# Kernel tuning notes

Hardware: AMD Instinct MI355X
Metric: run time of the kernel (lower is better)

The kernel has to match this reference:

```python
import jax, jax.numpy as jnp
import numpy as np
from jax import lax

BATCH = 524288
N_LINKS = 8   # body 0 = fixed base, bodies 1..7 have revolute joints
N_DOFS = 7
G = 9.81      # base linear acceleration z-component encodes gravity

def _skew(v):
    x, y, z = v[..., 0], v[..., 1], v[..., 2]
    o = jnp.zeros_like(x)
    return jnp.stack([jnp.stack([o, -z, y], -1),
                      jnp.stack([z, o, -x], -1),
                      jnp.stack([-y, x, o], -1)], -2)

def _rodrigues(axis, theta):
    # rotation about unit axis by theta; broadcasts axis[...,3] with theta[...]
    K = _skew(axis)
    s = jnp.sin(theta)[..., None, None]
    c = jnp.cos(theta)[..., None, None]
    I = jnp.eye(3, dtype=jnp.result_type(theta))
    return I + s * K + (1.0 - c) * (K @ K)

def setup_inputs():
    key = jax.random.key(0)
    ks = jax.random.split(key, 10)
    q = jax.random.normal(ks[0], (BATCH, N_DOFS), jnp.float32)
    qd = jax.random.normal(ks[1], (BATCH, N_DOFS), jnp.float32)
    qdd_des = jax.random.normal(ks[2], (BATCH, N_DOFS), jnp.float32)
    # fixed (URDF) joint transforms: valid random rotations + link-offset translations
    ax = jax.random.normal(ks[3], (N_LINKS, 3), jnp.float32)
    ax = ax / jnp.linalg.norm(ax, axis=-1, keepdims=True)
    ang = jax.random.uniform(ks[4], (N_LINKS,), jnp.float32, -1.0, 1.0)
    rot_fix = _rodrigues(ax, ang)
    trans_fix = jax.random.uniform(ks[5], (N_LINKS, 3), jnp.float32, -0.25, 0.25)
    # single-coordinate joint axes with signs, as in URDF revolute joints
    joint_axes = jnp.asarray([[0, 0, 1], [0, 1, 0], [0, 0, 1], [0, -1, 0],
                              [0, 0, 1], [0, 1, 0], [0, 0, 1]], jnp.float32)
    mass = jax.random.uniform(ks[6], (N_LINKS,), jnp.float32, 0.5, 4.0)
    com = 0.05 * jax.random.normal(ks[7], (N_LINKS, 3), jnp.float32)
    A = 0.1 * jax.random.normal(ks[8], (N_LINKS, 3, 3), jnp.float32)
    inertia = A @ jnp.swapaxes(A, -1, -2) + 0.05 * jnp.eye(3, dtype=jnp.float32)
    damping = jax.random.uniform(ks[9], (N_DOFS,), jnp.float32, 0.01, 0.2)
    return dict(q=q, qd=qd, qdd_des=qdd_des, rot_fix=rot_fix, trans_fix=trans_fix,
                joint_axes=joint_axes, mass=mass, com=com, inertia=inertia, damping=damping)

def reference(q, qd, qdd_des, rot_fix, trans_fix, joint_axes, mass, com, inertia, damping):
    # Batched recursive Newton-Euler inverse dynamics over a serial chain,
    # matching DifferentiableRobotModel.compute_inverse_dynamics (gravity+damping on).
    B, D = q.shape
    # joint pose of body i(=dof j+1): rotation = rot_fix[i] @ R(axis_j, q_j), translation = trans_fix[i]
    Rq = _rodrigues(joint_axes[None, :, :], q)                     # [B,D,3,3]
    R = jnp.einsum('dij,bdjk->dbik', rot_fix[1:], Rq)              # [D,B,3,3]
    p = trans_fix[1:]                                              # [D,3]
    jv = qd.T[:, :, None] * joint_axes[:, None, :]                 # [D,B,3] joint angular vel
    ja = qdd_des.T[:, :, None] * joint_axes[:, None, :]            # [D,B,3] joint angular acc

    z = jnp.zeros((B, 3), q.dtype)
    base_acc_lin = z.at[:, 2].set(G)

    # forward pass: propagate spatial velocity/acceleration root -> leaf
    def fwd_step(carry, xs):
        vl, va, al, aa = carry
        Ri, pi, jvi, jai = xs
        Rt = jnp.swapaxes(Ri, -1, -2)
        pinv = -jnp.einsum('bij,j->bi', Rt, pi)
        # SpatialMotionVec.transform with inverse joint pose (Rt, pinv)
        va_n = jnp.einsum('bij,bj->bi', Rt, va)
        vl_n = jnp.einsum('bij,bj->bi', Rt, vl) + jnp.cross(pinv, va_n)
        va_i = va_n + jvi
        vl_i = vl_n
        aa_n = jnp.einsum('bij,bj->bi', Rt, aa)
        al_n = jnp.einsum('bij,bj->bi', Rt, al) + jnp.cross(pinv, aa_n)
        # acc = parent_acc(transformed) + joint_acc + vel x joint_vel (joint_vel.lin = 0)
        aa_i = aa_n + jai + jnp.cross(va_i, jvi)
        al_i = al_n + jnp.cross(vl_i, jvi)
        new = (vl_i, va_i, al_i, aa_i)
        return new, new

    _, (vl, va, al, aa) = lax.scan(fwd_step, (z, z, base_acc_lin, z), (R, p, jv, ja))

    # spatial inertia (about body frame origin) acting on motion vectors
    m = mass[1:, None, None]                                       # [D,1,1]
    mc = mass[1:, None] * com[1:]                                  # [D,3]
    cs = _skew(com[1:])
    Io = inertia[1:] + mass[1:, None, None] * (cs @ jnp.swapaxes(cs, -1, -2))

    def imul(lin, ang):
        return (m * lin + jnp.cross(ang, mc[:, None, :]),
                jnp.einsum('dij,dbj->dbi', Io, ang) + jnp.cross(mc[:, None, :], lin))

    Ia_l, Ia_a = imul(al, aa)
    Iv_l, Iv_a = imul(vl, va)
    # f = I*acc + vel x* (I*vel)
    f_l = Ia_l + jnp.cross(va, Iv_l)
    f_a = Ia_a + jnp.cross(va, Iv_a) + jnp.cross(vl, Iv_l)

    # backward pass: accumulate forces leaf -> root; tau_j = f.ang . axis_j
    def bwd_step(carry, xs):
        cl, ca = carry
        fl, fa, Ri, pi, axi = xs
        tl = fl + cl
        ta = fa + ca
        tau = jnp.einsum('bi,i->b', ta, axi)
        # SpatialForceVec.transform with joint pose (Ri, pi)
        nl = jnp.einsum('bij,bj->bi', Ri, tl)
        na = jnp.einsum('bij,bj->bi', Ri, ta) + jnp.cross(pi[None, :], nl)
        return (nl, na), tau

    _, taus = lax.scan(bwd_step, (z, z), (f_l, f_a, R, p, joint_axes), reverse=True)
    return jnp.swapaxes(taus, 0, 1) + damping[None, :] * qd        # [B,D]
```

## Files before the change

kernel.cpp:

```cpp
#include <hip/hip_runtime.h>

#define NDOF 7
#define BLK 256
#define CST_STRIDE 24
#define CST_TOT (NDOF * CST_STRIDE)

struct V3 { float x, y, z; };
__device__ __forceinline__ V3 operator+(V3 a, V3 b) { return {a.x + b.x, a.y + b.y, a.z + b.z}; }
__device__ __forceinline__ V3 operator-(V3 a, V3 b) { return {a.x - b.x, a.y - b.y, a.z - b.z}; }
__device__ __forceinline__ V3 operator*(float s, V3 a) { return {s * a.x, s * a.y, s * a.z}; }
__device__ __forceinline__ V3 cross(V3 a, V3 b) {
    return {a.y * b.z - a.z * b.y, a.z * b.x - a.x * b.z, a.x * b.y - a.y * b.x};
}
__device__ __forceinline__ float dot(V3 a, V3 b) { return a.x * b.x + a.y * b.y + a.z * b.z; }

__global__ void rnea_prep(const float* __restrict__ rot_fix,
                          const float* __restrict__ trans_fix,
                          const float* __restrict__ mass_g,
                          const float* __restrict__ com_g,
                          const float* __restrict__ inertia_g,
                          const float* __restrict__ damping_g,
                          float* __restrict__ cst) {
    const int d = threadIdx.x;
    if (d >= NDOF) return;
    float* o = cst + d * CST_STRIDE;
    const float* F = rot_fix + (1 + d) * 9;
#pragma unroll
    for (int j = 0; j < 3; j++)
#pragma unroll
        for (int i = 0; i < 3; i++) o[j * 3 + i] = F[i * 3 + j];
#pragma unroll
    for (int i = 0; i < 3; i++) o[9 + i] = trans_fix[(1 + d) * 3 + i];
    const float m = mass_g[1 + d];
    const float c0 = com_g[(1 + d) * 3 + 0];
    const float c1 = com_g[(1 + d) * 3 + 1];
    const float c2 = com_g[(1 + d) * 3 + 2];
    const float* I = inertia_g + (1 + d) * 9;
    o[12] = I[0] + m * (c1 * c1 + c2 * c2);
    o[13] = I[1] - m * c0 * c1;
    o[14] = I[2] - m * c0 * c2;
    o[15] = I[4] + m * (c0 * c0 + c2 * c2);
    o[16] = I[5] - m * c1 * c2;
    o[17] = I[8] + m * (c0 * c0 + c1 * c1);
    o[18] = m;
    o[19] = m * c0;
    o[20] = m * c1;
    o[21] = m * c2;
    o[22] = damping_g[d];
    o[23] = 0.f;
}

template <int AX>
__device__ __forceinline__ void make_R(V3 Fc0, V3 Fc1, V3 Fc2, float s, float c,
                                       V3& R0, V3& R1, V3& R2) {
    if (AX == 0) {
        R0 = c * Fc0 + s * Fc1;
        R1 = c * Fc1 - s * Fc0;
        R2 = Fc2;
    } else if (AX == 1) {
        R0 = c * Fc0 - s * Fc2;
        R1 = Fc1;
        R2 = s * Fc0 + c * Fc2;
    } else {
        R0 = c * Fc0 + s * Fc2;
        R1 = Fc1;
        R2 = c * Fc2 - s * Fc0;
    }
}

template <int AX>
__device__ __forceinline__ void fwd_step(const float* __restrict__ C, float s, float c,
                                         float qd, float qdd, V3& vl, V3& va, V3& al,
                                         V3& aa, V3& fl, V3& fa) {
    const V3 Fc0{C[0], C[1], C[2]};
    const V3 Fc1{C[3], C[4], C[5]};
    const V3 Fc2{C[6], C[7], C[8]};
    const V3 p{C[9], C[10], C[11]};
    const float I00 = C[12], I01 = C[13], I02 = C[14], I11 = C[15], I12 = C[16], I22 = C[17];
    const float m = C[18];
    const V3 mc{C[19], C[20], C[21]};

    V3 R0, R1, R2;
    make_R<AX>(Fc0, Fc1, Fc2, s, c, R0, R1, R2);

    V3 w1 = vl + cross(va, p);
    V3 w2 = al + cross(aa, p);
    V3 nvl{dot(R0, w1), dot(R1, w1), dot(R2, w1)};
    V3 nva{dot(R0, va), dot(R1, va), dot(R2, va)};
    V3 nal{dot(R0, w2), dot(R1, w2), dot(R2, w2)};
    V3 naa{dot(R0, aa), dot(R1, aa), dot(R2, aa)};

    if (AX == 0) {
        va = {nva.x, nva.y, nva.z + qd};
        aa = {naa.x + va.y * qd, naa.y - va.x * qd, naa.z + qdd};
        vl = nvl;
        al = {nal.x + vl.y * qd, nal.y - vl.x * qd, nal.z};
    } else if (AX == 1) {
        va = {nva.x, nva.y + qd, nva.z};
        aa = {naa.x - va.z * qd, naa.y + qdd, naa.z + va.x * qd};
        vl = nvl;
        al = {nal.x - vl.z * qd, nal.y, nal.z + vl.x * qd};
    } else {
        va = {nva.x, nva.y - qd, nva.z};
        aa = {naa.x + va.z * qd, naa.y - qdd, naa.z - va.x * qd};
        vl = nvl;
        al = {nal.x + vl.z * qd, nal.y, nal.z - vl.x * qd};
    }

    V3 Ial = m * al + cross(aa, mc);
    V3 Iaa = V3{I00 * aa.x + I01 * aa.y + I02 * aa.z,
                I01 * aa.x + I11 * aa.y + I12 * aa.z,
                I02 * aa.x + I12 * aa.y + I22 * aa.z} + cross(mc, al);
    V3 Ivl = m * vl + cross(va, mc);
    V3 Iva = V3{I00 * va.x + I01 * va.y + I02 * va.z,
                I01 * va.x + I11 * va.y + I12 * va.z,
                I02 * va.x + I12 * va.y + I22 * va.z} + cross(mc, vl);
    fl = Ial + cross(va, Ivl);
    fa = Iaa + cross(va, Iva) + cross(vl, Ivl);
}

template <int AX>
__device__ __forceinline__ float bwd_core(const float* __restrict__ C, float s, float c,
                                          V3 fl, V3 fa, V3& cl, V3& ca) {
    const V3 Fc0{C[0], C[1], C[2]};
    const V3 Fc1{C[3], C[4], C[5]};
    const V3 Fc2{C[6], C[7], C[8]};
    const V3 p{C[9], C[10], C[11]};

    V3 tl = fl + cl;
    V3 ta = fa + ca;
    float tau;
    if (AX == 0) tau = ta.z;
    else if (AX == 1) tau = ta.y;
    else tau = -ta.y;

    V3 R0, R1, R2;
    make_R<AX>(Fc0, Fc1, Fc2, s, c, R0, R1, R2);
    V3 nl = tl.x * R0 + tl.y * R1 + tl.z * R2;
    V3 na = ta.x * R0 + ta.y * R1 + ta.z * R2 + cross(p, nl);
    cl = nl;
    ca = na;
    return tau;
}

__global__ __launch_bounds__(BLK) void rnea_main(
    const float* __restrict__ q_g, const float* __restrict__ qd_g,
    const float* __restrict__ qdd_g, const float* __restrict__ cst,
    float* __restrict__ out, int nbatch) {
    const int t = threadIdx.x;
    const int row = blockIdx.x * BLK + t;
    const int rowc = row < nbatch ? row : (nbatch - 1);
    const size_t go = (size_t)rowc * NDOF;

    float q[NDOF], qd[NDOF], qdd[NDOF], ss[NDOF], cc[NDOF];
#pragma unroll
    for (int d = 0; d < NDOF; d++) q[d] = q_g[go + d];
#pragma unroll
    for (int d = 0; d < NDOF; d++) qd[d] = qd_g[go + d];
#pragma unroll
    for (int d = 0; d < NDOF; d++) qdd[d] = qdd_g[go + d];
#pragma unroll
    for (int d = 0; d < NDOF; d++) { ss[d] = __sinf(q[d]); cc[d] = __cosf(q[d]); }

    V3 vl{0.f, 0.f, 0.f}, va{0.f, 0.f, 0.f}, al{0.f, 0.f, 9.81f}, aa{0.f, 0.f, 0.f};
    V3 fl0, fa0, fl1, fa1, fl2, fa2, fl3, fa3, fl4, fa4, fl5, fa5, fl6, fa6;

    fwd_step<0>(cst + 0 * CST_STRIDE, ss[0], cc[0], qd[0], qdd[0], vl, va, al, aa, fl0, fa0);
    fwd_step<1>(cst + 1 * CST_STRIDE, ss[1], cc[1], qd[1], qdd[1], vl, va, al, aa, fl1, fa1);
    fwd_step<0>(cst + 2 * CST_STRIDE, ss[2], cc[2], qd[2], qdd[2], vl, va, al, aa, fl2, fa2);
    fwd_step<2>(cst + 3 * CST_STRIDE, ss[3], cc[3], qd[3], qdd[3], vl, va, al, aa, fl3, fa3);
    fwd_step<0>(cst + 4 * CST_STRIDE, ss[4], cc[4], qd[4], qdd[4], vl, va, al, aa, fl4, fa4);
    fwd_step<1>(cst + 5 * CST_STRIDE, ss[5], cc[5], qd[5], qdd[5], vl, va, al, aa, fl5, fa5);
    fwd_step<0>(cst + 6 * CST_STRIDE, ss[6], cc[6], qd[6], qdd[6], vl, va, al, aa, fl6, fa6);

    V3 cl{0.f, 0.f, 0.f}, ca{0.f, 0.f, 0.f};
    float tau[NDOF];
    tau[6] = bwd_core<0>(cst + 6 * CST_STRIDE, ss[6], cc[6], fl6, fa6, cl, ca);
    tau[5] = bwd_core<1>(cst + 5 * CST_STRIDE, ss[5], cc[5], fl5, fa5, cl, ca);
    tau[4] = bwd_core<0>(cst + 4 * CST_STRIDE, ss[4], cc[4], fl4, fa4, cl, ca);
    tau[3] = bwd_core<2>(cst + 3 * CST_STRIDE, ss[3], cc[3], fl3, fa3, cl, ca);
    tau[2] = bwd_core<0>(cst + 2 * CST_STRIDE, ss[2], cc[2], fl2, fa2, cl, ca);
    tau[1] = bwd_core<1>(cst + 1 * CST_STRIDE, ss[1], cc[1], fl1, fa1, cl, ca);
    tau[0] = bwd_core<0>(cst + 0 * CST_STRIDE, ss[0], cc[0], fl0, fa0, cl, ca);

    if (row < nbatch) {
#pragma unroll
        for (int d = 0; d < NDOF; d++)
            out[go + d] = tau[d] + cst[d * CST_STRIDE + 22] * qd[d];
    }
}

extern "C" void kernel_launch(void* const* d_in, const int* in_sizes, int n_in,
                              void* d_out, int out_size, void* d_ws, size_t ws_size,
                              hipStream_t stream) {
    const float* q = (const float*)d_in[0];
    const float* qd = (const float*)d_in[1];
    const float* qdd = (const float*)d_in[2];
    const float* rot_fix = (const float*)d_in[3];
    const float* trans_fix = (const float*)d_in[4];
    const float* mass = (const float*)d_in[6];
    const float* com = (const float*)d_in[7];
    const float* inertia = (const float*)d_in[8];
    const float* damping = (const float*)d_in[9];
    float* out = (float*)d_out;
    float* cst = (float*)d_ws;

    const int n_elem = in_sizes[0];
    const int B = n_elem / NDOF;
    const int grid = (B + BLK - 1) / BLK;

    rnea_prep<<<1, 64, 0, stream>>>(rot_fix, trans_fix, mass, com, inertia, damping, cst);
    rnea_main<<<grid, BLK, 0, stream>>>(q, qd, qdd, cst, out, B);
}
```

Before: 134.5 us.

## Stage per-row inputs and outputs through shared memory with coalesced float4 copies

Each block now loads its contiguous slab of q, qd and qdd into shared memory using float4 vector loads, then each thread reads its 7-element row from LDS. Outputs are written back to shared memory and stored with coalesced float4 writes. This replaces the strided 7-float per-thread global accesses, which coalesce poorly, at the cost of about 21 KB of LDS per block, extra barriers, and stride-7 LDS reads.

```diff
diff --git a/kernel.cpp b/kernel.cpp
--- a/kernel.cpp
+++ b/kernel.cpp
@@ -4,6 +4,8 @@
 #define BLK 256
 #define CST_STRIDE 24
 #define CST_TOT (NDOF * CST_STRIDE)
+#define BELEM (BLK * NDOF)
+#define BVEC (BELEM / 4)
 
 struct V3 { float x, y, z; };
 __device__ __forceinline__ V3 operator+(V3 a, V3 b) { return {a.x + b.x, a.y + b.y, a.z + b.z}; }
@@ -147,20 +149,51 @@
     const float* __restrict__ q_g, const float* __restrict__ qd_g,
     const float* __restrict__ qdd_g, const float* __restrict__ cst,
     float* __restrict__ out, int nbatch) {
+    __shared__ __align__(16) float sQ[BELEM];
+    __shared__ __align__(16) float sQd[BELEM];
+    __shared__ __align__(16) float sQdd[BELEM];
     const int t = threadIdx.x;
-    const int row = blockIdx.x * BLK + t;
-    const int rowc = row < nbatch ? row : (nbatch - 1);
-    const size_t go = (size_t)rowc * NDOF;
-
-    float q[NDOF], qd[NDOF], qdd[NDOF], ss[NDOF], cc[NDOF];
-#pragma unroll
-    for (int d = 0; d < NDOF; d++) q[d] = q_g[go + d];
-#pragma unroll
-    for (int d = 0; d < NDOF; d++) qd[d] = qd_g[go + d];
-#pragma unroll
-    for (int d = 0; d < NDOF; d++) qdd[d] = qdd_g[go + d];
-#pragma unroll
-    for (int d = 0; d < NDOF; d++) { ss[d] = __sinf(q[d]); cc[d] = __cosf(q[d]); }
+    const int row0 = blockIdx.x * BLK;
+    const size_t base = (size_t)row0 * NDOF;
+    const bool full = (row0 + BLK) <= nbatch;
+
+    if (full) {
+        const float4* gq = reinterpret_cast<const float4*>(q_g + base);
+        const float4* gqd = reinterpret_cast<const float4*>(qd_g + base);
+        const float4* gqdd = reinterpret_cast<const float4*>(qdd_g + base);
+        float4* s4q = reinterpret_cast<float4*>(sQ);
+        float4* s4qd = reinterpret_cast<float4*>(sQd);
+        float4* s4qdd = reinterpret_cast<float4*>(sQdd);
+#pragma unroll
+        for (int i = 0; i < 2; i++) {
+            const int idx = t + i * BLK;
+            if (idx < BVEC) {
+                s4q[idx] = gq[idx];
+                s4qd[idx] = gqd[idx];
+                s4qdd[idx] = gqdd[idx];
+            }
+        }
+    } else {
+        const int totalE = nbatch * NDOF;
+        for (int i = t; i < BELEM; i += BLK) {
+            const size_t gi = base + i;
+            const bool in = gi < (size_t)totalE;
+            sQ[i] = in ? q_g[gi] : 0.f;
+            sQd[i] = in ? qd_g[gi] : 0.f;
+            sQdd[i] = in ? qdd_g[gi] : 0.f;
+        }
+    }
+    __syncthreads();
+
+    float qd[NDOF], qdd[NDOF], ss[NDOF], cc[NDOF];
+#pragma unroll
+    for (int d = 0; d < NDOF; d++) {
+        const float qv = sQ[t * NDOF + d];
+        ss[d] = __sinf(qv);
+        cc[d] = __cosf(qv);
+        qd[d] = sQd[t * NDOF + d];
+        qdd[d] = sQdd[t * NDOF + d];
+    }
 
     V3 vl{0.f, 0.f, 0.f}, va{0.f, 0.f, 0.f}, al{0.f, 0.f, 9.81f}, aa{0.f, 0.f, 0.f};
     V3 fl0, fa0, fl1, fa1, fl2, fa2, fl3, fa3, fl4, fa4, fl5, fa5, fl6, fa6;
@@ -183,10 +216,26 @@
     tau[1] = bwd_core<1>(cst + 1 * CST_STRIDE, ss[1], cc[1], fl1, fa1, cl, ca);
     tau[0] = bwd_core<0>(cst + 0 * CST_STRIDE, ss[0], cc[0], fl0, fa0, cl, ca);
 
-    if (row < nbatch) {
-#pragma unroll
-        for (int d = 0; d < NDOF; d++)
-            out[go + d] = tau[d] + cst[d * CST_STRIDE + 22] * qd[d];
+    __syncthreads();
+#pragma unroll
+    for (int d = 0; d < NDOF; d++)
+        sQ[t * NDOF + d] = tau[d] + cst[d * CST_STRIDE + 22] * qd[d];
+    __syncthreads();
+
+    if (full) {
+        const float4* s4 = reinterpret_cast<const float4*>(sQ);
+        float4* g4 = reinterpret_cast<float4*>(out + base);
+#pragma unroll
+        for (int i = 0; i < 2; i++) {
+            const int idx = t + i * BLK;
+            if (idx < BVEC) g4[idx] = s4[idx];
+        }
+    } else {
+        const int totalE = nbatch * NDOF;
+        for (int i = t; i < BELEM; i += BLK) {
+            const size_t gi = base + i;
+            if (gi < (size_t)totalE) out[gi] = sQ[i];
+        }
     }
 }
 
```

New measurement: 141.0 us. 1.05x slower.

## Process two rows per thread with packed f32x2 math and LDS-parked forces

Applied to the files above, without the earlier changes.

Each thread now handles two batch rows using float2 ext vectors, so the arithmetic can map to packed FP32 instructions. Per-link forces for the first five links are parked in shared memory instead of registers, and the forward and backward passes become non-unrolled loops. This lowers register pressure and code size. Constants are staged in LDS and loaded as float4, and q/qd are reloaded and sin/cos recomputed in the backward pass. It trades extra LDS traffic, recomputation and loop overhead for packed math and lower register use.

```diff
diff --git a/kernel.cpp b/kernel.cpp
--- a/kernel.cpp
+++ b/kernel.cpp
@@ -1,18 +1,26 @@
 #include <hip/hip_runtime.h>
 
 #define NDOF 7
-#define BLK 256
+#define NPARK 5
+#define BLK 128
+#define RPB 256
 #define CST_STRIDE 24
 #define CST_TOT (NDOF * CST_STRIDE)
-
-struct V3 { float x, y, z; };
-__device__ __forceinline__ V3 operator+(V3 a, V3 b) { return {a.x + b.x, a.y + b.y, a.z + b.z}; }
-__device__ __forceinline__ V3 operator-(V3 a, V3 b) { return {a.x - b.x, a.y - b.y, a.z - b.z}; }
-__device__ __forceinline__ V3 operator*(float s, V3 a) { return {s * a.x, s * a.y, s * a.z}; }
-__device__ __forceinline__ V3 cross(V3 a, V3 b) {
+#define SF_V2 (NPARK * 6 * BLK)
+
+typedef float f32x2 __attribute__((ext_vector_type(2)));
+
+__device__ __forceinline__ f32x2 splat(float v) { f32x2 r; r.x = v; r.y = v; return r; }
+
+struct PV3 { f32x2 x, y, z; };
+__device__ __forceinline__ PV3 operator+(PV3 a, PV3 b) { return {a.x + b.x, a.y + b.y, a.z + b.z}; }
+__device__ __forceinline__ PV3 operator-(PV3 a, PV3 b) { return {a.x - b.x, a.y - b.y, a.z - b.z}; }
+__device__ __forceinline__ PV3 operator*(f32x2 s, PV3 a) { return {s * a.x, s * a.y, s * a.z}; }
+__device__ __forceinline__ PV3 cross(PV3 a, PV3 b) {
     return {a.y * b.z - a.z * b.y, a.z * b.x - a.x * b.z, a.x * b.y - a.y * b.x};
 }
-__device__ __forceinline__ float dot(V3 a, V3 b) { return a.x * b.x + a.y * b.y + a.z * b.z; }
+__device__ __forceinline__ f32x2 dot(PV3 a, PV3 b) { return a.x * b.x + a.y * b.y + a.z * b.z; }
+__device__ __forceinline__ PV3 uv(float x, float y, float z) { return {splat(x), splat(y), splat(z)}; }
 
 __global__ void rnea_prep(const float* __restrict__ rot_fix,
                           const float* __restrict__ trans_fix,
@@ -51,8 +59,8 @@
 }
 
 template <int AX>
-__device__ __forceinline__ void make_R(V3 Fc0, V3 Fc1, V3 Fc2, float s, float c,
-                                       V3& R0, V3& R1, V3& R2) {
+__device__ __forceinline__ void make_R(PV3 Fc0, PV3 Fc1, PV3 Fc2, f32x2 s, f32x2 c,
+                                       PV3& R0, PV3& R1, PV3& R2) {
     if (AX == 0) {
         R0 = c * Fc0 + s * Fc1;
         R1 = c * Fc1 - s * Fc0;
@@ -69,26 +77,28 @@
 }
 
 template <int AX>
-__device__ __forceinline__ void fwd_step(const float* __restrict__ C, float s, float c,
-                                         float qd, float qdd, V3& vl, V3& va, V3& al,
-                                         V3& aa, V3& fl, V3& fa) {
-    const V3 Fc0{C[0], C[1], C[2]};
-    const V3 Fc1{C[3], C[4], C[5]};
-    const V3 Fc2{C[6], C[7], C[8]};
-    const V3 p{C[9], C[10], C[11]};
-    const float I00 = C[12], I01 = C[13], I02 = C[14], I11 = C[15], I12 = C[16], I22 = C[17];
-    const float m = C[18];
-    const V3 mc{C[19], C[20], C[21]};
-
-    V3 R0, R1, R2;
+__device__ __forceinline__ void fwd_step(float4 A0, float4 A1, float4 A2, float4 A3,
+                                         float4 A4, float4 A5, f32x2 s, f32x2 c,
+                                         f32x2 qd, f32x2 qdd, PV3& vl, PV3& va, PV3& al,
+                                         PV3& aa, PV3& fl, PV3& fa) {
+    const PV3 Fc0 = uv(A0.x, A0.y, A0.z);
+    const PV3 Fc1 = uv(A0.w, A1.x, A1.y);
+    const PV3 Fc2 = uv(A1.z, A1.w, A2.x);
+    const PV3 p = uv(A2.y, A2.z, A2.w);
+    const f32x2 I00 = splat(A3.x), I01 = splat(A3.y), I02 = splat(A3.z);
+    const f32x2 I11 = splat(A3.w), I12 = splat(A4.x), I22 = splat(A4.y);
+    const f32x2 m = splat(A4.z);
+    const PV3 mc = uv(A4.w, A5.x, A5.y);
+
+    PV3 R0, R1, R2;
     make_R<AX>(Fc0, Fc1, Fc2, s, c, R0, R1, R2);
 
-    V3 w1 = vl + cross(va, p);
-    V3 w2 = al + cross(aa, p);
-    V3 nvl{dot(R0, w1), dot(R1, w1), dot(R2, w1)};
-    V3 nva{dot(R0, va), dot(R1, va), dot(R2, va)};
-    V3 nal{dot(R0, w2), dot(R1, w2), dot(R2, w2)};
-    V3 naa{dot(R0, aa), dot(R1, aa), dot(R2, aa)};
+    PV3 w1 = vl + cross(va, p);
+    PV3 w2 = al + cross(aa, p);
+    PV3 nvl{dot(R0, w1), dot(R1, w1), dot(R2, w1)};
+    PV3 nva{dot(R0, va), dot(R1, va), dot(R2, va)};
+    PV3 nal{dot(R0, w2), dot(R1, w2), dot(R2, w2)};
+    PV3 naa{dot(R0, aa), dot(R1, aa), dot(R2, aa)};
 
     if (AX == 0) {
         va = {nva.x, nva.y, nva.z + qd};
@@ -107,86 +117,152 @@
         al = {nal.x + vl.z * qd, nal.y, nal.z - vl.x * qd};
     }
 
-    V3 Ial = m * al + cross(aa, mc);
-    V3 Iaa = V3{I00 * aa.x + I01 * aa.y + I02 * aa.z,
-                I01 * aa.x + I11 * aa.y + I12 * aa.z,
-                I02 * aa.x + I12 * aa.y + I22 * aa.z} + cross(mc, al);
-    V3 Ivl = m * vl + cross(va, mc);
-    V3 Iva = V3{I00 * va.x + I01 * va.y + I02 * va.z,
-                I01 * va.x + I11 * va.y + I12 * va.z,
-                I02 * va.x + I12 * va.y + I22 * va.z} + cross(mc, vl);
+    PV3 Ial = m * al + cross(aa, mc);
+    PV3 Iaa = PV3{I00 * aa.x + I01 * aa.y + I02 * aa.z,
+                  I01 * aa.x + I11 * aa.y + I12 * aa.z,
+                  I02 * aa.x + I12 * aa.y + I22 * aa.z} + cross(mc, al);
+    PV3 Ivl = m * vl + cross(va, mc);
+    PV3 Iva = PV3{I00 * va.x + I01 * va.y + I02 * va.z,
+                  I01 * va.x + I11 * va.y + I12 * va.z,
+                  I02 * va.x + I12 * va.y + I22 * va.z} + cross(mc, vl);
     fl = Ial + cross(va, Ivl);
     fa = Iaa + cross(va, Iva) + cross(vl, Ivl);
 }
 
 template <int AX>
-__device__ __forceinline__ float bwd_core(const float* __restrict__ C, float s, float c,
-                                          V3 fl, V3 fa, V3& cl, V3& ca) {
-    const V3 Fc0{C[0], C[1], C[2]};
-    const V3 Fc1{C[3], C[4], C[5]};
-    const V3 Fc2{C[6], C[7], C[8]};
-    const V3 p{C[9], C[10], C[11]};
-
-    V3 tl = fl + cl;
-    V3 ta = fa + ca;
-    float tau;
+__device__ __forceinline__ f32x2 bwd_core(float4 A0, float4 A1, float4 A2,
+                                          f32x2 s, f32x2 c,
+                                          PV3 fl, PV3 fa, PV3& cl, PV3& ca) {
+    const PV3 Fc0 = uv(A0.x, A0.y, A0.z);
+    const PV3 Fc1 = uv(A0.w, A1.x, A1.y);
+    const PV3 Fc2 = uv(A1.z, A1.w, A2.x);
+    const PV3 p = uv(A2.y, A2.z, A2.w);
+
+    PV3 tl = fl + cl;
+    PV3 ta = fa + ca;
+    f32x2 tau;
     if (AX == 0) tau = ta.z;
     else if (AX == 1) tau = ta.y;
-    else tau = -ta.y;
-
-    V3 R0, R1, R2;
+    else tau = splat(0.f) - ta.y;
+
+    PV3 R0, R1, R2;
     make_R<AX>(Fc0, Fc1, Fc2, s, c, R0, R1, R2);
-    V3 nl = tl.x * R0 + tl.y * R1 + tl.z * R2;
-    V3 na = ta.x * R0 + ta.y * R1 + ta.z * R2 + cross(p, nl);
+    PV3 nl = tl.x * R0 + tl.y * R1 + tl.z * R2;
+    PV3 na = ta.x * R0 + ta.y * R1 + ta.z * R2 + cross(p, nl);
     cl = nl;
     ca = na;
     return tau;
 }
+
+__device__ __forceinline__ int axid(int d) { return (d & 1) ? ((d == 3) ? 2 : 1) : 0; }
 
 __global__ __launch_bounds__(BLK) void rnea_main(
     const float* __restrict__ q_g, const float* __restrict__ qd_g,
     const float* __restrict__ qdd_g, const float* __restrict__ cst,
     float* __restrict__ out, int nbatch) {
+    __shared__ __align__(16) float sC[CST_TOT];
+    __shared__ f32x2 sF[SF_V2];
     const int t = threadIdx.x;
-    const int row = blockIdx.x * BLK + t;
-    const int rowc = row < nbatch ? row : (nbatch - 1);
-    const size_t go = (size_t)rowc * NDOF;
-
-    float q[NDOF], qd[NDOF], qdd[NDOF], ss[NDOF], cc[NDOF];
-#pragma unroll
-    for (int d = 0; d < NDOF; d++) q[d] = q_g[go + d];
-#pragma unroll
-    for (int d = 0; d < NDOF; d++) qd[d] = qd_g[go + d];
-#pragma unroll
-    for (int d = 0; d < NDOF; d++) qdd[d] = qdd_g[go + d];
-#pragma unroll
-    for (int d = 0; d < NDOF; d++) { ss[d] = __sinf(q[d]); cc[d] = __cosf(q[d]); }
-
-    V3 vl{0.f, 0.f, 0.f}, va{0.f, 0.f, 0.f}, al{0.f, 0.f, 9.81f}, aa{0.f, 0.f, 0.f};
-    V3 fl0, fa0, fl1, fa1, fl2, fa2, fl3, fa3, fl4, fa4, fl5, fa5, fl6, fa6;
-
-    fwd_step<0>(cst + 0 * CST_STRIDE, ss[0], cc[0], qd[0], qdd[0], vl, va, al, aa, fl0, fa0);
-    fwd_step<1>(cst + 1 * CST_STRIDE, ss[1], cc[1], qd[1], qdd[1], vl, va, al, aa, fl1, fa1);
-    fwd_step<0>(cst + 2 * CST_STRIDE, ss[2], cc[2], qd[2], qdd[2], vl, va, al, aa, fl2, fa2);
-    fwd_step<2>(cst + 3 * CST_STRIDE, ss[3], cc[3], qd[3], qdd[3], vl, va, al, aa, fl3, fa3);
-    fwd_step<0>(cst + 4 * CST_STRIDE, ss[4], cc[4], qd[4], qdd[4], vl, va, al, aa, fl4, fa4);
-    fwd_step<1>(cst + 5 * CST_STRIDE, ss[5], cc[5], qd[5], qdd[5], vl, va, al, aa, fl5, fa5);
-    fwd_step<0>(cst + 6 * CST_STRIDE, ss[6], cc[6], qd[6], qdd[6], vl, va, al, aa, fl6, fa6);
-
-    V3 cl{0.f, 0.f, 0.f}, ca{0.f, 0.f, 0.f};
-    float tau[NDOF];
-    tau[6] = bwd_core<0>(cst + 6 * CST_STRIDE, ss[6], cc[6], fl6, fa6, cl, ca);
-    tau[5] = bwd_core<1>(cst + 5 * CST_STRIDE, ss[5], cc[5], fl5, fa5, cl, ca);
-    tau[4] = bwd_core<0>(cst + 4 * CST_STRIDE, ss[4], cc[4], fl4, fa4, cl, ca);
-    tau[3] = bwd_core<2>(cst + 3 * CST_STRIDE, ss[3], cc[3], fl3, fa3, cl, ca);
-    tau[2] = bwd_core<0>(cst + 2 * CST_STRIDE, ss[2], cc[2], fl2, fa2, cl, ca);
-    tau[1] = bwd_core<1>(cst + 1 * CST_STRIDE, ss[1], cc[1], fl1, fa1, cl, ca);
-    tau[0] = bwd_core<0>(cst + 0 * CST_STRIDE, ss[0], cc[0], fl0, fa0, cl, ca);
-
-    if (row < nbatch) {
-#pragma unroll
-        for (int d = 0; d < NDOF; d++)
-            out[go + d] = tau[d] + cst[d * CST_STRIDE + 22] * qd[d];
+    const int rowA = blockIdx.x * RPB + t;
+    const int rowB = rowA + BLK;
+    const bool okA = rowA < nbatch;
+    const bool okB = rowB < nbatch;
+    const int rcA = okA ? rowA : (nbatch - 1);
+    const int rcB = okB ? rowB : (nbatch - 1);
+    const size_t goA = (size_t)rcA * NDOF;
+    const size_t goB = (size_t)rcB * NDOF;
+
+    if (t < CST_TOT / 4)
+        reinterpret_cast<float4*>(sC)[t] = reinterpret_cast<const float4*>(cst)[t];
+    __syncthreads();
+
+    PV3 vl{splat(0.f), splat(0.f), splat(0.f)};
+    PV3 va = vl, aa = vl;
+    PV3 al{splat(0.f), splat(0.f), splat(9.81f)};
+    f32x2 qn, qdn, qddn;
+    qn.x = q_g[goA];   qn.y = q_g[goB];
+    qdn.x = qd_g[goA]; qdn.y = qd_g[goB];
+    qddn.x = qdd_g[goA]; qddn.y = qdd_g[goB];
+#pragma clang loop unroll(disable)
+    for (int d = 0; d < NPARK; ++d) {
+        const f32x2 q = qn, qd = qdn, qdd = qddn;
+        qn.x = q_g[goA + d + 1];   qn.y = q_g[goB + d + 1];
+        qdn.x = qd_g[goA + d + 1]; qdn.y = qd_g[goB + d + 1];
+        qddn.x = qdd_g[goA + d + 1]; qddn.y = qdd_g[goB + d + 1];
+        f32x2 s, c;
+        s.x = __sinf(q.x); s.y = __sinf(q.y);
+        c.x = __cosf(q.x); c.y = __cosf(q.y);
+        const float4* C4 = reinterpret_cast<const float4*>(sC) + d * 6;
+        const float4 A0 = C4[0], A1 = C4[1], A2 = C4[2], A3 = C4[3], A4 = C4[4], A5 = C4[5];
+        PV3 fl, fa;
+        switch (axid(d)) {
+            case 0: fwd_step<0>(A0, A1, A2, A3, A4, A5, s, c, qd, qdd, vl, va, al, aa, fl, fa); break;
+            case 1: fwd_step<1>(A0, A1, A2, A3, A4, A5, s, c, qd, qdd, vl, va, al, aa, fl, fa); break;
+            default: fwd_step<2>(A0, A1, A2, A3, A4, A5, s, c, qd, qdd, vl, va, al, aa, fl, fa); break;
+        }
+        f32x2* r = sF + d * 6 * BLK + t;
+        r[0 * BLK] = fl.x; r[1 * BLK] = fl.y; r[2 * BLK] = fl.z;
+        r[3 * BLK] = fa.x; r[4 * BLK] = fa.y; r[5 * BLK] = fa.z;
+    }
+
+    const f32x2 q5 = qn, qd5 = qdn, qdd5 = qddn;
+    f32x2 q6, qd6, qdd6;
+    q6.x = q_g[goA + 6];   q6.y = q_g[goB + 6];
+    qd6.x = qd_g[goA + 6]; qd6.y = qd_g[goB + 6];
+    qdd6.x = qdd_g[goA + 6]; qdd6.y = qdd_g[goB + 6];
+    f32x2 s5, c5, s6, c6;
+    s5.x = __sinf(q5.x); s5.y = __sinf(q5.y);
+    c5.x = __cosf(q5.x); c5.y = __cosf(q5.y);
+    s6.x = __sinf(q6.x); s6.y = __sinf(q6.y);
+    c6.x = __cosf(q6.x); c6.y = __cosf(q6.y);
+    PV3 cl{splat(0.f), splat(0.f), splat(0.f)}, ca = cl;
+    f32x2 tau5, tau6;
+    {
+        const float4* C5 = reinterpret_cast<const float4*>(sC) + 5 * 6;
+        const float4 B0 = C5[0], B1 = C5[1], B2 = C5[2], B3 = C5[3], B4 = C5[4], B5 = C5[5];
+        const float4* C6 = reinterpret_cast<const float4*>(sC) + 6 * 6;
+        const float4 D0 = C6[0], D1 = C6[1], D2 = C6[2], D3 = C6[3], D4 = C6[4], D5 = C6[5];
+        PV3 fl5, fa5, fl6, fa6;
+        fwd_step<1>(B0, B1, B2, B3, B4, B5, s5, c5, qd5, qdd5, vl, va, al, aa, fl5, fa5);
+        fwd_step<0>(D0, D1, D2, D3, D4, D5, s6, c6, qd6, qdd6, vl, va, al, aa, fl6, fa6);
+        tau6 = bwd_core<0>(D0, D1, D2, s6, c6, fl6, fa6, cl, ca) + splat(D5.z) * qd6;
+        tau5 = bwd_core<1>(B0, B1, B2, s5, c5, fl5, fa5, cl, ca) + splat(B5.z) * qd5;
+    }
+
+#pragma clang loop unroll(disable)
+    for (int d = NPARK - 1; d >= 0; --d) {
+        f32x2 q, qd;
+        q.x = q_g[goA + d];  q.y = q_g[goB + d];
+        qd.x = qd_g[goA + d]; qd.y = qd_g[goB + d];
+        f32x2 s, c;
+        s.x = __sinf(q.x); s.y = __sinf(q.y);
+        c.x = __cosf(q.x); c.y = __cosf(q.y);
+        const float4* C4 = reinterpret_cast<const float4*>(sC) + d * 6;
+        const float4 A0 = C4[0], A1 = C4[1], A2 = C4[2];
+        const float damp = sC[d * CST_STRIDE + 22];
+        f32x2* r = sF + d * 6 * BLK + t;
+        const PV3 fl{r[0 * BLK], r[1 * BLK], r[2 * BLK]};
+        const PV3 fa{r[3 * BLK], r[4 * BLK], r[5 * BLK]};
+        f32x2 tau;
+        switch (axid(d)) {
+            case 0: tau = bwd_core<0>(A0, A1, A2, s, c, fl, fa, cl, ca); break;
+            case 1: tau = bwd_core<1>(A0, A1, A2, s, c, fl, fa, cl, ca); break;
+            default: tau = bwd_core<2>(A0, A1, A2, s, c, fl, fa, cl, ca); break;
+        }
+        r[0] = tau + splat(damp) * qd;
+    }
+
+    if (okA) {
+#pragma unroll
+        for (int d = 0; d < NPARK; ++d) out[goA + d] = sF[d * 6 * BLK + t].x;
+        out[goA + 5] = tau5.x;
+        out[goA + 6] = tau6.x;
+    }
+    if (okB) {
+#pragma unroll
+        for (int d = 0; d < NPARK; ++d) out[goB + d] = sF[d * 6 * BLK + t].y;
+        out[goB + 5] = tau5.y;
+        out[goB + 6] = tau6.y;
     }
 }
 
@@ -207,7 +283,7 @@
 
     const int n_elem = in_sizes[0];
     const int B = n_elem / NDOF;
-    const int grid = (B + BLK - 1) / BLK;
+    const int grid = (B + RPB - 1) / RPB;
 
     rnea_prep<<<1, 64, 0, stream>>>(rot_fix, trans_fix, mass, com, inertia, damping, cst);
     rnea_main<<<grid, BLK, 0, stream>>>(q, qd, qdd, cst, out, B);
```

New measurement: 118.9 us, median of 2. -11.6%, faster.
